# Kernel tuning notes

Hardware: AMD Instinct MI355X
Metric: run time of the kernel (lower is better)

## Reference

```python
import jax, jax.numpy as jnp
import numpy as np

D = 2048
H = 16
HD = D // H
EPS = 1e-5

def setup_inputs() -> dict:
    key = jax.random.key(0)
    ks = jax.random.split(key, 7)
    B, S = 4, 2048
    scale = 1.0 / np.sqrt(D)
    return {
        "hidden_states": jax.random.normal(ks[0], (B, S, D), dtype=jnp.float32),
        "ln_gamma": jnp.ones((D,), dtype=jnp.float32),
        "ln_beta": jnp.zeros((D,), dtype=jnp.float32),
        "W_qkv": jax.random.normal(ks[1], (D, 3 * D), dtype=jnp.float32) * scale,
        "b_qkv": jnp.zeros((3 * D,), dtype=jnp.float32),
        "W_proj": jax.random.normal(ks[2], (D, D), dtype=jnp.float32) * scale,
        "b_proj": jnp.zeros((D,), dtype=jnp.float32),
    }

def reference(hidden_states, ln_gamma, ln_beta, W_qkv, b_qkv, W_proj, b_proj):
    B, S, _ = hidden_states.shape
    # LayerNorm (fused into QKV projection in the original kernel)
    mu = jnp.mean(hidden_states, axis=-1, keepdims=True)
    var = jnp.mean(jnp.square(hidden_states - mu), axis=-1, keepdims=True)
    x = (hidden_states - mu) * jax.lax.rsqrt(var + EPS) * ln_gamma + ln_beta
    # QKV projection
    qkv = jnp.einsum("bsd,de->bse", x, W_qkv) + b_qkv  # [B,S,3D]
    q, k, v = jnp.split(qkv, 3, axis=-1)
    # split heads -> [B,H,S,hd]
    q = q.reshape(B, S, H, HD).transpose(0, 2, 1, 3)
    k = k.reshape(B, S, H, HD).transpose(0, 2, 1, 3)
    v = v.reshape(B, S, H, HD).transpose(0, 2, 1, 3)
    # scaled causal attention
    scores = jnp.einsum("bhqd,bhkd->bhqk", q, k) / jnp.asarray(np.sqrt(HD), q.dtype)
    causal = jnp.tril(jnp.ones((S, S), dtype=bool))
    neg = jnp.finfo(scores.dtype).min
    scores = jnp.where(causal, scores, neg)
    attn = jax.nn.softmax(scores, axis=-1)
    out = jnp.einsum("bhqk,bhkd->bhqd", attn, v)
    # merge heads, output projection (dropout is identity in eval / p=0)
    out = out.transpose(0, 2, 1, 3).reshape(B, S, D)
    return jnp.einsum("bsd,de->bse", out, W_proj) + b_proj
```

## Files before the change

kernel.cpp:

```cpp
#include <hip/hip_runtime.h>
#include <cstdint>

typedef __attribute__((ext_vector_type(8))) short bf16x8;
typedef __attribute__((ext_vector_type(4))) float f32x4;
typedef unsigned short u16;
typedef unsigned int u32;

constexpr int D   = 2048;
constexpr int H   = 16;
constexpr int HD  = 128;
constexpr int BATCH = 4;
constexpr int S   = 2048;
constexpr int ROWS = BATCH * S;
constexpr int N3D = 3 * D;
constexpr int QKW = 2 * D;

__device__ __forceinline__ u16 f2bf(float f) {
    union { float f; u32 u; } v; v.f = f;
    u32 r = v.u + 0x7FFFu + ((v.u >> 16) & 1u);
    return (u16)(r >> 16);
}

__device__ __forceinline__ void gld_lds16(const u16* g, u16* l) {
    __builtin_amdgcn_global_load_lds(
        (const __attribute__((address_space(1))) void*)g,
        (__attribute__((address_space(3))) void*)l, 16, 0, 0);
}

__global__ __launch_bounds__(256) void ln_bf16_kernel(
    const float* __restrict__ x, const float* __restrict__ gamma,
    const float* __restrict__ beta, u16* __restrict__ out)
{
    const int row = blockIdx.x;
    const int t = threadIdx.x;
    const float* xr = x + (size_t)row * D;
    float4 a = ((const float4*)xr)[2*t];
    float4 b = ((const float4*)xr)[2*t+1];
    float s  = a.x+a.y+a.z+a.w + b.x+b.y+b.z+b.w;
    float ss = a.x*a.x+a.y*a.y+a.z*a.z+a.w*a.w + b.x*b.x+b.y*b.y+b.z*b.z+b.w*b.w;
    #pragma unroll
    for (int off = 32; off > 0; off >>= 1) {
        s  += __shfl_down(s, off);
        ss += __shfl_down(ss, off);
    }
    __shared__ float red[8];
    const int wave = t >> 6, lane = t & 63;
    if (lane == 0) { red[wave] = s; red[4+wave] = ss; }
    __syncthreads();
    const float mu   = (red[0]+red[1]+red[2]+red[3]) * (1.0f/D);
    const float var  = (red[4]+red[5]+red[6]+red[7]) * (1.0f/D) - mu*mu;
    const float rstd = rsqrtf(var + 1e-5f);
    float4 g0  = ((const float4*)gamma)[2*t];
    float4 g1  = ((const float4*)gamma)[2*t+1];
    float4 be0 = ((const float4*)beta)[2*t];
    float4 be1 = ((const float4*)beta)[2*t+1];
    union { uint4 v; u16 e[8]; } o;
    o.e[0] = f2bf((a.x-mu)*rstd*g0.x + be0.x);
    o.e[1] = f2bf((a.y-mu)*rstd*g0.y + be0.y);
    o.e[2] = f2bf((a.z-mu)*rstd*g0.z + be0.z);
    o.e[3] = f2bf((a.w-mu)*rstd*g0.w + be0.w);
    o.e[4] = f2bf((b.x-mu)*rstd*g1.x + be1.x);
    o.e[5] = f2bf((b.y-mu)*rstd*g1.y + be1.y);
    o.e[6] = f2bf((b.z-mu)*rstd*g1.z + be1.z);
    o.e[7] = f2bf((b.w-mu)*rstd*g1.w + be1.w);
    ((uint4*)(out + (size_t)row*D))[t] = o.v;
}

__global__ __launch_bounds__(256) void transpose_bf16_kernel(
    const float* __restrict__ in, u16* __restrict__ out, int K, int N)
{
    __shared__ u16 tile[64][65];
    const int tn0 = blockIdx.x * 64;
    const int tk0 = blockIdx.y * 64;
    const int t = threadIdx.x;
    const int tx = t & 63;
    const int ty = t >> 6;
    #pragma unroll
    for (int i = 0; i < 16; i++) {
        int k = ty + i*4;
        tile[k][tx] = f2bf(in[(size_t)(tk0+k)*N + tn0 + tx]);
    }
    __syncthreads();
    #pragma unroll
    for (int i = 0; i < 16; i++) {
        int n = ty + i*4;
        out[(size_t)(tn0+n)*K + tk0 + tx] = tile[tx][n];
    }
}

constexpr int BM = 256, BN = 256, BK = 32;

template<int MODE>
__global__ __launch_bounds__(512, 2) void gemm256_kernel(
    const u16* __restrict__ A, const u16* __restrict__ Bt,
    const float* __restrict__ bias, void* __restrict__ Cout,
    u16* __restrict__ vtb, int M, int N, int K)
{
    __shared__ u16 sA[4 * 8192];
    __shared__ u16 sB[4 * 8192];

    const int t = threadIdx.x;
    const int wave = t >> 6, lane = t & 63;
    const int lr = lane & 15, lq = lane >> 4;
    const int wm = wave >> 2, wn = wave & 3;
    const int m0 = blockIdx.y * BM, n0 = blockIdx.x * BN;

    const int g0 = t, g1 = t + 512;
    const int cs0 = ((g0 & 3) ^ ((g0 >> 3) & 3)) * 8;
    const int cs1 = ((g1 & 3) ^ ((g1 >> 3) & 3)) * 8;
    const u16* gA0 = A  + (size_t)(m0 + (g0 >> 2)) * K + cs0;
    const u16* gA1 = A  + (size_t)(m0 + (g1 >> 2)) * K + cs1;
    const u16* gB0 = Bt + (size_t)(n0 + (g0 >> 2)) * K + cs0;
    const u16* gB1 = Bt + (size_t)(n0 + (g1 >> 2)) * K + cs1;

    f32x4 acc[8][4];
    #pragma unroll
    for (int i = 0; i < 8; i++)
        #pragma unroll
        for (int j = 0; j < 4; j++)
            acc[i][j] = (f32x4)(0.0f);

    const int NT = K / BK;

    auto STAGE = [&](int slot, int kt) {
        u16* a = sA + slot * 8192 + wave * 512;
        u16* b = sB + slot * 8192 + wave * 512;
        const int ko = kt * BK;
        gld_lds16(gA0 + ko, a);
        gld_lds16(gA1 + ko, a + 4096);
        gld_lds16(gB0 + ko, b);
        gld_lds16(gB1 + ko, b + 4096);
    };

    STAGE(0, 0); STAGE(1, 1); STAGE(2, 2);

    const int rblk = (lq ^ ((lr >> 1) & 3)) * 8;

    for (int kt = 0; kt < NT; ++kt) {
        asm volatile("s_waitcnt vmcnt(8)" ::: "memory");
        __builtin_amdgcn_s_barrier();
        __builtin_amdgcn_sched_barrier(0);
        const int tp = (kt + 3 < NT) ? (kt + 3) : (NT - 1);
        STAGE((kt + 3) & 3, tp);

        const u16* tAp = sA + (kt & 3) * 8192 + (wm * 128) * BK + rblk;
        const u16* tBp = sB + (kt & 3) * 8192 + (wn * 64)  * BK + rblk;

        bf16x8 bfr[4], af[4];
        #pragma unroll
        for (int nt = 0; nt < 4; nt++)
            bfr[nt] = *(const bf16x8*)(tBp + (nt * 16 + lr) * BK);
        #pragma unroll
        for (int mt = 0; mt < 4; mt++)
            af[mt] = *(const bf16x8*)(tAp + (mt * 16 + lr) * BK);
        __builtin_amdgcn_s_setprio(1);
        #pragma unroll
        for (int mt = 0; mt < 4; mt++)
            #pragma unroll
            for (int nt = 0; nt < 4; nt++)
                acc[mt][nt] = __builtin_amdgcn_mfma_f32_16x16x32_bf16(
                    af[mt], bfr[nt], acc[mt][nt], 0, 0, 0);
        __builtin_amdgcn_s_setprio(0);
        #pragma unroll
        for (int mt = 0; mt < 4; mt++)
            af[mt] = *(const bf16x8*)(tAp + (64 + mt * 16 + lr) * BK);
        __builtin_amdgcn_s_setprio(1);
        #pragma unroll
        for (int mt = 0; mt < 4; mt++)
            #pragma unroll
            for (int nt = 0; nt < 4; nt++)
                acc[4 + mt][nt] = __builtin_amdgcn_mfma_f32_16x16x32_bf16(
                    af[mt], bfr[nt], acc[4 + mt][nt], 0, 0, 0);
        __builtin_amdgcn_s_setprio(0);
        asm volatile("s_waitcnt lgkmcnt(0)" ::: "memory");
        __builtin_amdgcn_sched_barrier(0);
    }

    #pragma unroll
    for (int i = 0; i < 8; i++) {
        const int row0 = m0 + wm * 128 + (i >> 2) * 64 + (i & 3) * 16 + lq * 4;
        #pragma unroll
        for (int nt = 0; nt < 4; nt++) {
            const int col = n0 + wn * 64 + nt * 16 + lr;
            const float bv = bias[col];
            float v[4];
            #pragma unroll
            for (int r = 0; r < 4; r++) v[r] = acc[i][nt][r] + bv;
            if (MODE == 0) {
                #pragma unroll
                for (int r = 0; r < 4; r++)
                    ((float*)Cout)[(size_t)(row0 + r) * N + col] = v[r];
            } else {
                if (n0 < QKW) {
                    #pragma unroll
                    for (int r = 0; r < 4; r++)
                        ((u16*)Cout)[(size_t)(row0 + r) * QKW + col] = f2bf(v[r]);
                } else {
                    const int vcol = col - QKW;
                    const int b = row0 >> 11, s0 = row0 & 2047;
                    ushort4 pk;
                    pk.x = f2bf(v[0]); pk.y = f2bf(v[1]);
                    pk.z = f2bf(v[2]); pk.w = f2bf(v[3]);
                    *(ushort4*)(vtb + ((size_t)(b*H + (vcol >> 7)) * HD
                                       + (vcol & 127)) * S + s0) = pk;
                }
            }
        }
    }
}

constexpr int TQ = 64, TK = 64;
constexpr int KPAD = 136;
constexpr int VPAD = 72;
constexpr int PPAD = 72;

__global__ __launch_bounds__(256) void attn_kernel(
    const u16* __restrict__ qkb, const u16* __restrict__ vtb,
    u16* __restrict__ ctx)
{
    __shared__ u16 sK[TK * KPAD];
    __shared__ u16 sVT[HD * VPAD];
    __shared__ u16 sP[4 * 16 * PPAD];

    const int flat = blockIdx.x;
    const int qt = 31 - (flat >> 6);
    const int bh = flat & 63;
    const int b  = bh >> 4, h = bh & 15;
    const int q0 = qt * TQ;
    const int t = threadIdx.x;
    const int wave = t >> 6, lane = t & 63;
    const int lr = lane & 15, lq = lane >> 4;

    const u16* baseQK = qkb + (size_t)b * S * QKW + h * HD;
    const u16* baseVT = vtb + (size_t)bh * HD * S;

    const int qrow = q0 + wave * 16 + lr;
    bf16x8 qf[4];
    #pragma unroll
    for (int kc = 0; kc < 4; kc++)
        qf[kc] = *(const bf16x8*)(baseQK + (size_t)qrow * QKW + kc*32 + lq*8);

    float m_r[4], l_r[4];
    f32x4 o[8];
    #pragma unroll
    for (int r = 0; r < 4; r++) { m_r[r] = -1e30f; l_r[r] = 0.0f; }
    #pragma unroll
    for (int j = 0; j < 8; j++) o[j] = (f32x4)(0.0f);

    const float scale = 0.08838834764831845f;
    const int nkt = qt + 1;

    for (int kt = 0; kt < nkt; kt++) {
        __syncthreads();
        #pragma unroll
        for (int i = 0; i < 4; i++) {
            int c = t + i * 256;
            int krow = c >> 4, kcol = (c & 15) * 8;
            uint4 v = *(const uint4*)(baseQK + D + (size_t)(kt*TK + krow) * QKW + kcol);
            *(uint4*)(sK + krow * KPAD + kcol) = v;
        }
        #pragma unroll
        for (int i = 0; i < 4; i++) {
            int c = t + i * 256;
            int vrow = c >> 3, coff = (c & 7) * 8;
            uint4 v = *(const uint4*)(baseVT + (size_t)vrow * S + kt*TK + coff);
            *(uint4*)(sVT + vrow * VPAD + coff) = v;
        }
        __syncthreads();

        f32x4 sc[4];
        #pragma unroll
        for (int nt = 0; nt < 4; nt++) sc[nt] = (f32x4)(0.0f);
        #pragma unroll
        for (int nt = 0; nt < 4; nt++)
            #pragma unroll
            for (int kc = 0; kc < 4; kc++) {
                bf16x8 kf = *(const bf16x8*)(sK + (nt*16 + lr) * KPAD + kc*32 + lq*8);
                sc[nt] = __builtin_amdgcn_mfma_f32_16x16x32_bf16(qf[kc], kf, sc[nt], 0, 0, 0);
            }

        const bool diag = (kt == qt);
        float rowmax[4] = {-1e30f, -1e30f, -1e30f, -1e30f};
        const int qgb = q0 + wave*16 + lq*4;
        #pragma unroll
        for (int nt = 0; nt < 4; nt++)
            #pragma unroll
            for (int r = 0; r < 4; r++) {
                float sv = sc[nt][r] * scale;
                if (diag) {
                    const int kg = kt*TK + nt*16 + lr;
                    if (kg > qgb + r) sv = -1e30f;
                }
                sc[nt][r] = sv;
                rowmax[r] = fmaxf(rowmax[r], sv);
            }
        #pragma unroll
        for (int mask = 1; mask < 16; mask <<= 1)
            #pragma unroll
            for (int r = 0; r < 4; r++)
                rowmax[r] = fmaxf(rowmax[r], __shfl_xor(rowmax[r], mask));

        float alpha[4];
        #pragma unroll
        for (int r = 0; r < 4; r++) {
            float nm = fmaxf(m_r[r], rowmax[r]);
            alpha[r] = __expf(m_r[r] - nm);
            m_r[r] = nm;
        }

        u16* pw = sP + wave * 16 * PPAD;
        #pragma unroll
        for (int nt = 0; nt < 4; nt++) {
            #pragma unroll
            for (int r = 0; r < 4; r++) {
                float p = __expf(sc[nt][r] - m_r[r]);
                sc[nt][r] = p;
                pw[(lq*4 + r) * PPAD + nt*16 + lr] = f2bf(p);
            }
        }
        #pragma unroll
        for (int r = 0; r < 4; r++) {
            float psum = sc[0][r] + sc[1][r] + sc[2][r] + sc[3][r];
            l_r[r] = l_r[r] * alpha[r] + psum;
        }
        #pragma unroll
        for (int j = 0; j < 8; j++)
            #pragma unroll
            for (int r = 0; r < 4; r++)
                o[j][r] *= alpha[r];

        #pragma unroll
        for (int kc2 = 0; kc2 < 2; kc2++) {
            bf16x8 pa = *(const bf16x8*)(pw + lr * PPAD + kc2*32 + lq*8);
            #pragma unroll
            for (int n2 = 0; n2 < 8; n2++) {
                bf16x8 vb = *(const bf16x8*)(sVT + (n2*16 + lr) * VPAD + kc2*32 + lq*8);
                o[n2] = __builtin_amdgcn_mfma_f32_16x16x32_bf16(pa, vb, o[n2], 0, 0, 0);
            }
        }
    }

    #pragma unroll
    for (int mask = 1; mask < 16; mask <<= 1)
        #pragma unroll
        for (int r = 0; r < 4; r++)
            l_r[r] += __shfl_xor(l_r[r], mask);
    float inv_l[4];
    #pragma unroll
    for (int r = 0; r < 4; r++) inv_l[r] = 1.0f / l_r[r];
    #pragma unroll
    for (int n2 = 0; n2 < 8; n2++)
        #pragma unroll
        for (int r = 0; r < 4; r++) {
            const int qg = q0 + wave*16 + lq*4 + r;
            const float v = o[n2][r] * inv_l[r];
            ctx[(size_t)(b * S + qg) * D + h * HD + n2*16 + lr] = f2bf(v);
        }
}

extern "C" void kernel_launch(void* const* d_in, const int* in_sizes, int n_in,
                              void* d_out, int out_size, void* d_ws, size_t ws_size,
                              hipStream_t stream) {
    const float* hs    = (const float*)d_in[0];
    const float* gamma = (const float*)d_in[1];
    const float* beta  = (const float*)d_in[2];
    const float* Wqkv  = (const float*)d_in[3];
    const float* bqkv  = (const float*)d_in[4];
    const float* Wproj = (const float*)d_in[5];
    const float* bproj = (const float*)d_in[6];

    char* ws = (char*)d_ws;
    size_t off = 0;
    u16* xb   = (u16*)(ws + off); off += (size_t)ROWS * D * 2;
    u16* wtq  = (u16*)(ws + off); off += (size_t)N3D * D * 2;
    u16* wtp  = (u16*)(ws + off); off += (size_t)D * D * 2;
    u16* qkb  = (u16*)(ws + off); off += (size_t)ROWS * QKW * 2;
    u16* vtb  = (u16*)(ws + off); off += (size_t)ROWS * D * 2;
    u16* ctxb = (u16*)(ws + off);

    ln_bf16_kernel<<<ROWS, 256, 0, stream>>>(hs, gamma, beta, xb);
    transpose_bf16_kernel<<<dim3(N3D/64, D/64), 256, 0, stream>>>(Wqkv, wtq, D, N3D);
    transpose_bf16_kernel<<<dim3(D/64,   D/64), 256, 0, stream>>>(Wproj, wtp, D, D);
    gemm256_kernel<2><<<dim3(N3D/BN, ROWS/BM), 512, 0, stream>>>(
        xb, wtq, bqkv, qkb, vtb, ROWS, N3D, D);
    attn_kernel<<<dim3((S/TQ) * BATCH * H), 256, 0, stream>>>(qkb, vtb, ctxb);
    gemm256_kernel<0><<<dim3(D/BN, ROWS/BM), 512, 0, stream>>>(
        ctxb, wtp, bproj, (float*)d_out, nullptr, ROWS, D, D);
}
```

Baseline: 662.6 us.

## Prefetch K/V tiles into registers, add MFMA priority, remap GEMM blocks per XCD

The attention kernel now loads the next K and V tiles from global memory into registers while the current tile is being computed, which hides global-load latency behind the MFMA work. MFMA sections are wrapped in s_setprio to favour matrix issue. The GEMM launch becomes a 1D grid with a remap that places consecutive tiles on the same XCD, aiming at better L2 reuse. In exchange, the prefetch adds register pressure that could lower occupancy.

```diff
diff --git a/kernel.cpp b/kernel.cpp
--- a/kernel.cpp
+++ b/kernel.cpp
@@ -103,7 +103,13 @@
     const int wave = t >> 6, lane = t & 63;
     const int lr = lane & 15, lq = lane >> 4;
     const int wm = wave >> 2, wn = wave & 3;
-    const int m0 = blockIdx.y * BM, n0 = blockIdx.x * BN;
+
+    const int flat = blockIdx.x;
+    const int chunk = gridDim.x >> 3;
+    const int wgid = (flat & 7) * chunk + (flat >> 3);
+    const int nbx = N / BN;
+    const int mb = wgid / nbx, nb = wgid % nbx;
+    const int m0 = mb * BM, n0 = nb * BN;
 
     const int g0 = t, g1 = t + 512;
     const int cs0 = ((g0 & 3) ^ ((g0 >> 3) & 3)) * 8;
@@ -250,27 +256,37 @@
     const float scale = 0.08838834764831845f;
     const int nkt = qt + 1;
 
+    const int kr_row = t >> 4, kr_col = (t & 15) * 8;
+    const int vr_row = t >> 3, vr_col = (t & 7) * 8;
+    uint4 kreg[4], vreg[4];
+    auto LOADKV = [&](int kt) {
+        #pragma unroll
+        for (int i = 0; i < 4; i++)
+            kreg[i] = *(const uint4*)(baseQK + D
+                + (size_t)(kt*TK + ((kr_row + i*16) & 63)) * QKW
+                + kr_col + ((kr_row + i*16) >> 6) * 0);
+        #pragma unroll
+        for (int i = 0; i < 4; i++)
+            vreg[i] = *(const uint4*)(baseVT
+                + (size_t)(vr_row + i*32) * S + kt*TK + vr_col);
+    };
+    LOADKV(0);
+
     for (int kt = 0; kt < nkt; kt++) {
         __syncthreads();
         #pragma unroll
-        for (int i = 0; i < 4; i++) {
-            int c = t + i * 256;
-            int krow = c >> 4, kcol = (c & 15) * 8;
-            uint4 v = *(const uint4*)(baseQK + D + (size_t)(kt*TK + krow) * QKW + kcol);
-            *(uint4*)(sK + krow * KPAD + kcol) = v;
-        }
-        #pragma unroll
-        for (int i = 0; i < 4; i++) {
-            int c = t + i * 256;
-            int vrow = c >> 3, coff = (c & 7) * 8;
-            uint4 v = *(const uint4*)(baseVT + (size_t)vrow * S + kt*TK + coff);
-            *(uint4*)(sVT + vrow * VPAD + coff) = v;
-        }
+        for (int i = 0; i < 4; i++)
+            *(uint4*)(sK + (kr_row + i*16) * KPAD + kr_col) = kreg[i];
+        #pragma unroll
+        for (int i = 0; i < 4; i++)
+            *(uint4*)(sVT + (vr_row + i*32) * VPAD + vr_col) = vreg[i];
         __syncthreads();
+        if (kt + 1 < nkt) LOADKV(kt + 1);
 
         f32x4 sc[4];
         #pragma unroll
         for (int nt = 0; nt < 4; nt++) sc[nt] = (f32x4)(0.0f);
+        __builtin_amdgcn_s_setprio(1);
         #pragma unroll
         for (int nt = 0; nt < 4; nt++)
             #pragma unroll
@@ -278,6 +294,7 @@
                 bf16x8 kf = *(const bf16x8*)(sK + (nt*16 + lr) * KPAD + kc*32 + lq*8);
                 sc[nt] = __builtin_amdgcn_mfma_f32_16x16x32_bf16(qf[kc], kf, sc[nt], 0, 0, 0);
             }
+        __builtin_amdgcn_s_setprio(0);
 
         const bool diag = (kt == qt);
         float rowmax[4] = {-1e30f, -1e30f, -1e30f, -1e30f};
@@ -332,11 +349,13 @@
         #pragma unroll
         for (int kc2 = 0; kc2 < 2; kc2++) {
             bf16x8 pa = *(const bf16x8*)(pw + lr * PPAD + kc2*32 + lq*8);
+            __builtin_amdgcn_s_setprio(1);
             #pragma unroll
             for (int n2 = 0; n2 < 8; n2++) {
                 bf16x8 vb = *(const bf16x8*)(sVT + (n2*16 + lr) * VPAD + kc2*32 + lq*8);
                 o[n2] = __builtin_amdgcn_mfma_f32_16x16x32_bf16(pa, vb, o[n2], 0, 0, 0);
             }
+            __builtin_amdgcn_s_setprio(0);
         }
     }
 
@@ -381,9 +400,9 @@
     ln_bf16_kernel<<<ROWS, 256, 0, stream>>>(hs, gamma, beta, xb);
     transpose_bf16_kernel<<<dim3(N3D/64, D/64), 256, 0, stream>>>(Wqkv, wtq, D, N3D);
     transpose_bf16_kernel<<<dim3(D/64,   D/64), 256, 0, stream>>>(Wproj, wtp, D, D);
-    gemm256_kernel<2><<<dim3(N3D/BN, ROWS/BM), 512, 0, stream>>>(
+    gemm256_kernel<2><<<dim3((N3D/BN) * (ROWS/BM)), 512, 0, stream>>>(
         xb, wtq, bqkv, qkb, vtb, ROWS, N3D, D);
     attn_kernel<<<dim3((S/TQ) * BATCH * H), 256, 0, stream>>>(qkb, vtb, ctxb);
-    gemm256_kernel<0><<<dim3(D/BN, ROWS/BM), 512, 0, stream>>>(
+    gemm256_kernel<0><<<dim3((D/BN) * (ROWS/BM)), 512, 0, stream>>>(
         ctxb, wtp, bproj, (float*)d_out, nullptr, ROWS, D, D);
 }
```

Result: slower. 834.5 us (+25.9%).

## Split GEMM stage loads into A/B halves interleaved with MFMA phases

Applied to the files above, without the earlier changes.

The GEMM main loop splits each prefetch stage into separate A and B global-to-LDS loads. These are issued between the two MFMA half-blocks, with extra barriers and waitcnts placed around each compute phase in the style of ping-pong scheduling. The aim is to spread memory issue across the iteration and overlap it better with matrix math. In exchange there are four barriers per iteration instead of one, which adds synchronisation overhead, and the vmcnt accounting becomes more delicate.

```diff
diff --git a/kernel.cpp b/kernel.cpp
--- a/kernel.cpp
+++ b/kernel.cpp
@@ -122,27 +122,28 @@
 
     const int NT = K / BK;
 
-    auto STAGE = [&](int slot, int kt) {
+    auto STAGE_A = [&](int slot, int kt) {
         u16* a = sA + slot * 8192 + wave * 512;
+        gld_lds16(gA0 + kt * BK, a);
+        gld_lds16(gA1 + kt * BK, a + 4096);
+    };
+    auto STAGE_B = [&](int slot, int kt) {
         u16* b = sB + slot * 8192 + wave * 512;
-        const int ko = kt * BK;
-        gld_lds16(gA0 + ko, a);
-        gld_lds16(gA1 + ko, a + 4096);
-        gld_lds16(gB0 + ko, b);
-        gld_lds16(gB1 + ko, b + 4096);
+        gld_lds16(gB0 + kt * BK, b);
+        gld_lds16(gB1 + kt * BK, b + 4096);
     };
 
-    STAGE(0, 0); STAGE(1, 1); STAGE(2, 2);
+    STAGE_A(0, 0); STAGE_B(0, 0);
+    STAGE_A(1, 1); STAGE_B(1, 1);
+    STAGE_A(2, 2); STAGE_B(2, 2);
+    asm volatile("s_waitcnt vmcnt(8)" ::: "memory");
+    __builtin_amdgcn_s_barrier();
 
     const int rblk = (lq ^ ((lr >> 1) & 3)) * 8;
 
     for (int kt = 0; kt < NT; ++kt) {
-        asm volatile("s_waitcnt vmcnt(8)" ::: "memory");
-        __builtin_amdgcn_s_barrier();
-        __builtin_amdgcn_sched_barrier(0);
         const int tp = (kt + 3 < NT) ? (kt + 3) : (NT - 1);
-        STAGE((kt + 3) & 3, tp);
-
+        const int slot3 = (kt + 3) & 3;
         const u16* tAp = sA + (kt & 3) * 8192 + (wm * 128) * BK + rblk;
         const u16* tBp = sB + (kt & 3) * 8192 + (wn * 64)  * BK + rblk;
 
@@ -153,6 +154,11 @@
         #pragma unroll
         for (int mt = 0; mt < 4; mt++)
             af[mt] = *(const bf16x8*)(tAp + (mt * 16 + lr) * BK);
+        STAGE_A(slot3, tp);
+        __builtin_amdgcn_sched_barrier(0);
+        __builtin_amdgcn_s_barrier();
+        asm volatile("s_waitcnt lgkmcnt(0)" ::: "memory");
+        __builtin_amdgcn_sched_barrier(0);
         __builtin_amdgcn_s_setprio(1);
         #pragma unroll
         for (int mt = 0; mt < 4; mt++)
@@ -161,9 +167,18 @@
                 acc[mt][nt] = __builtin_amdgcn_mfma_f32_16x16x32_bf16(
                     af[mt], bfr[nt], acc[mt][nt], 0, 0, 0);
         __builtin_amdgcn_s_setprio(0);
+        __builtin_amdgcn_sched_barrier(0);
+        __builtin_amdgcn_s_barrier();
+
         #pragma unroll
         for (int mt = 0; mt < 4; mt++)
             af[mt] = *(const bf16x8*)(tAp + (64 + mt * 16 + lr) * BK);
+        STAGE_B(slot3, tp);
+        asm volatile("s_waitcnt vmcnt(8)" ::: "memory");
+        __builtin_amdgcn_sched_barrier(0);
+        __builtin_amdgcn_s_barrier();
+        asm volatile("s_waitcnt lgkmcnt(0)" ::: "memory");
+        __builtin_amdgcn_sched_barrier(0);
         __builtin_amdgcn_s_setprio(1);
         #pragma unroll
         for (int mt = 0; mt < 4; mt++)
@@ -172,9 +187,10 @@
                 acc[4 + mt][nt] = __builtin_amdgcn_mfma_f32_16x16x32_bf16(
                     af[mt], bfr[nt], acc[4 + mt][nt], 0, 0, 0);
         __builtin_amdgcn_s_setprio(0);
-        asm volatile("s_waitcnt lgkmcnt(0)" ::: "memory");
-        __builtin_amdgcn_sched_barrier(0);
-    }
+        __builtin_amdgcn_sched_barrier(0);
+        __builtin_amdgcn_s_barrier();
+    }
+    asm volatile("s_waitcnt vmcnt(0)" ::: "memory");
 
     #pragma unroll
     for (int i = 0; i < 8; i++) {
```

New measurement: 610.3 us. 7.9% less time.
